# Optimization experiments

Hardware: AMD Instinct MI355X
Metric: run time of the kernel (lower is better)

## Reference

```python
import jax, jax.numpy as jnp
import numpy as np

ALPHA = 0.2  # LeakyReLU negative slope


def setup_inputs() -> dict:
    key = jax.random.key(0)
    ks = jax.random.split(key, 6)
    B, N, F_IN, F_OUT = 4, 4096, 128, 128
    return {
        "input": jax.random.normal(ks[0], (B, N, F_IN), dtype=jnp.float32),
        "adj": jax.random.uniform(ks[1], (B, N, N), dtype=jnp.float32),
        "W": jax.random.normal(ks[2], (F_IN, F_OUT), dtype=jnp.float32) * (np.sqrt(2.0) / np.sqrt(F_IN)),
        "a1": jax.random.normal(ks[3], (F_OUT, 1), dtype=jnp.float32) * 0.1,
        "a2": jax.random.normal(ks[4], (F_OUT, 1), dtype=jnp.float32) * 0.1,
        "bias": jax.random.normal(ks[5], (N, F_OUT), dtype=jnp.float32) * 0.02,
    }


def reference(input, adj, W, a1, a2, bias):
    # h = X @ W : [B, N, F_out]
    h = jnp.einsum("bnf,fo->bno", input, W)
    # additive attention scores: e[b,i,j] = leakyrelu(f1[b,i] + f2[b,j])
    f1 = h @ a1            # [B, N, 1]
    f2 = h @ a2            # [B, N, 1]
    e = f1 + jnp.swapaxes(f2, 1, 2)        # [B, N, N]
    e = jnp.where(e >= 0, e, ALPHA * e)    # LeakyReLU
    # NOTE: original multiplies adj into scores (not -inf masking) and
    # softmaxes over dim=1 (the first node axis), faithfully reproduced.
    attention = jax.nn.softmax(adj * e, axis=1)  # [B, N, N]
    # dropout p=0 / eval mode -> identity
    h_prime = jnp.einsum("bij,bjo->bio", attention, h) + bias[None, :, :]
    # in_features == out_features -> plain residual
    return h_prime + input
```

## Files before the change

kernel.cpp:

```cpp
#include <hip/hip_runtime.h>
#include <hip/hip_bf16.h>

typedef short short8 __attribute__((ext_vector_type(8)));
typedef float f32x4 __attribute__((ext_vector_type(4)));
typedef unsigned short u16;
typedef u16 u16x4 __attribute__((ext_vector_type(4)));
typedef u16 u16x8 __attribute__((ext_vector_type(8)));

static constexpr float kAlpha = 0.2f;

static __device__ inline u16 f2bf(float f) {
  __hip_bfloat16 h = __float2bfloat16(f);
  return *reinterpret_cast<u16*>(&h);
}
static __device__ inline float bf2f(u16 v) {
  unsigned int u = ((unsigned int)v) << 16;
  return __uint_as_float(u);
}

__global__ __launch_bounds__(256) void k1_hW(const float* __restrict__ X,
                                             const float* __restrict__ W,
                                             const float* __restrict__ a1,
                                             const float* __restrict__ a2,
                                             u16* __restrict__ hbT,
                                             float* __restrict__ f1,
                                             float* __restrict__ f2) {
  int row0 = blockIdx.x * 8;
  int o = threadIdx.x & 127;
  int g = threadIdx.x >> 7;
  __shared__ float Xs[8][128];
#pragma unroll
  for (int s = 0; s < 4; ++s) {
    int idx = threadIdx.x + s * 256;
    Xs[idx >> 7][idx & 127] = X[(size_t)row0 * 128 + idx];
  }
  __syncthreads();
  float acc[4] = {0.f, 0.f, 0.f, 0.f};
  for (int k = 0; k < 128; ++k) {
    float w = W[k * 128 + o];
#pragma unroll
    for (int s = 0; s < 4; ++s) acc[s] += Xs[g + 2 * s][k] * w;
  }
  int b = row0 >> 12;
  int n0 = row0 & 4095;
#pragma unroll
  for (int s = 0; s < 4; ++s)
    hbT[((size_t)b * 128 + o) * 4096 + n0 + g + 2 * s] = f2bf(acc[s]);

  float a1o = a1[o], a2o = a2[o];
  __syncthreads();
#pragma unroll
  for (int s = 0; s < 4; ++s) Xs[g + 2 * s][o] = acc[s] * a1o;
  __syncthreads();
  int r = threadIdx.x >> 5, c = threadIdx.x & 31;
  float s1 = Xs[r][c] + Xs[r][c + 32] + Xs[r][c + 64] + Xs[r][c + 96];
  s1 += __shfl_xor(s1, 1);
  s1 += __shfl_xor(s1, 2);
  s1 += __shfl_xor(s1, 4);
  s1 += __shfl_xor(s1, 8);
  s1 += __shfl_xor(s1, 16);
  if (c == 0) f1[b * 4096 + n0 + r] = s1;
  __syncthreads();
#pragma unroll
  for (int s = 0; s < 4; ++s) Xs[g + 2 * s][o] = acc[s] * a2o;
  __syncthreads();
  float s2 = Xs[r][c] + Xs[r][c + 32] + Xs[r][c + 64] + Xs[r][c + 96];
  s2 += __shfl_xor(s2, 1);
  s2 += __shfl_xor(s2, 2);
  s2 += __shfl_xor(s2, 4);
  s2 += __shfl_xor(s2, 8);
  s2 += __shfl_xor(s2, 16);
  if (c == 0) f2[b * 4096 + n0 + r] = s2;
}

__global__ __launch_bounds__(256) void k2_dpart(const float* __restrict__ adj,
                                                const float* __restrict__ f1,
                                                const float* __restrict__ f2,
                                                float* __restrict__ dpart) {
  int bid = blockIdx.x;
  int ic = bid & 31;
  int jt = (bid >> 5) & 15;
  int b = bid >> 9;
  int t = threadIdx.x;
  int c = t & 63, r = t >> 6;
  int j = jt * 256 + c * 4;
  const size_t badj = (size_t)b * 4096 * 4096;
  f32x4 f2v = *reinterpret_cast<const f32x4*>(&f2[b * 4096 + j]);
  const float* f1p = f1 + b * 4096;
  int row0 = ic * 128 + r;
  f32x4 sum = (f32x4){0.f, 0.f, 0.f, 0.f};
#pragma unroll 8
  for (int s = 0; s < 32; ++s) {
    int row = row0 + 4 * s;
    f32x4 a = *reinterpret_cast<const f32x4*>(&adj[badj + (size_t)row * 4096 + j]);
    float f1r = f1p[row];
#pragma unroll
    for (int k = 0; k < 4; ++k) {
      float e = f1r + f2v[k];
      e = e >= 0.f ? e : kAlpha * e;
      sum[k] += __expf(a[k] * e);
    }
  }
  __shared__ f32x4 red[256];
  red[t] = sum;
  __syncthreads();
  if (t < 64) {
    f32x4 tt = red[t] + red[t + 64] + red[t + 128] + red[t + 192];
    *reinterpret_cast<f32x4*>(&dpart[(size_t)(b * 32 + ic) * 4096 + j]) = tt;
  }
}

#define LROWW 72
#define BARRIER()                                      \
  {                                                    \
    asm volatile("s_waitcnt lgkmcnt(0)" ::: "memory"); \
    __builtin_amdgcn_s_barrier();                      \
  }
__global__ __launch_bounds__(512) void k3w(const float* __restrict__ adj,
                                           const u16* __restrict__ hbT,
                                           const float* __restrict__ f1,
                                           const float* __restrict__ f2,
                                           const float* __restrict__ dpart,
                                           u16* __restrict__ parts) {
  int bid0 = blockIdx.x;
  int bid = ((bid0 & 7) << 5) | (bid0 >> 3);
  int b = bid >> 6;
  int it = (bid >> 2) & 15;
  int jq = bid & 3;
  int i0 = it * 256;
  int jbase = jq * 1024;
  int t = threadIdx.x;
  int lane = t & 63;
  int w = t >> 6;
  int rw = w & 3;
  int cw = w >> 2;

  __shared__ u16 As[2][256 * LROWW];
  __shared__ u16 Bs[2][128 * LROWW];
  __shared__ float rds[1024];

  const size_t badj = (size_t)b * 4096 * 4096;
  const u16* hb = hbT + (size_t)b * 128 * 4096;
  const float* f2b = f2 + b * 4096;

  int r0 = t >> 4;
  int c0 = (t & 15) * 4;
  int bo = t >> 2;
  int bc0 = (t & 3) * 16;

  float f1v[8];
#pragma unroll
  for (int u = 0; u < 8; ++u) f1v[u] = f1[b * 4096 + i0 + r0 + 32 * u];

  int l15 = lane & 15;
  int l8 = (lane >> 4) * 8;

  f32x4 acc[4][4];
#pragma unroll
  for (int rg = 0; rg < 4; ++rg)
#pragma unroll
    for (int n = 0; n < 4; ++n) acc[rg][n] = (f32x4){0.f, 0.f, 0.f, 0.f};

  const float* ap0 = adj + badj + (size_t)(i0 + r0) * 4096 + c0;

  f32x4 raA0, raA1, raA2, raA3, raA4, raA5, raA6, raA7;
  f32x4 raB0, raB1, raB2, raB3, raB4, raB5, raB6, raB7;
  f32x4 rfA, rfB;
  u16x8 rbA0, rbA1, rbB0, rbB1;

#define PF(S, JO)                                                         \
  {                                                                       \
    int jj = jbase + ((JO) & 1023);    \
    const float* ap = ap0 + jj;                                           \
    ra##S##0 = *reinterpret_cast<const f32x4*>(ap);                       \
    ra##S##1 = *reinterpret_cast<const f32x4*>(ap + (size_t)1 * 131072);  \
    ra##S##2 = *reinterpret_cast<const f32x4*>(ap + (size_t)2 * 131072);  \
    ra##S##3 = *reinterpret_cast<const f32x4*>(ap + (size_t)3 * 131072);  \
    ra##S##4 = *reinterpret_cast<const f32x4*>(ap + (size_t)4 * 131072);  \
    ra##S##5 = *reinterpret_cast<const f32x4*>(ap + (size_t)5 * 131072);  \
    ra##S##6 = *reinterpret_cast<const f32x4*>(ap + (size_t)6 * 131072);  \
    ra##S##7 = *reinterpret_cast<const f32x4*>(ap + (size_t)7 * 131072);  \
    rf##S = *reinterpret_cast<const f32x4*>(f2b + jj + c0);               \
    const u16* bp = hb + (size_t)bo * 4096 + jj + bc0;                    \
    rb##S##0 = *reinterpret_cast<const u16x8*>(bp);                       \
    rb##S##1 = *reinterpret_cast<const u16x8*>(bp + 8);                   \
  }

#define STU(S, U, BUF)                                                    \
  {                                                                       \
    u16x4 pv;                                                             \
    _Pragma("unroll") for (int k = 0; k < 4; ++k) {                       \
      float e = f1v[U] + rf##S[k];                                        \
      e = e >= 0.f ? e : kAlpha * e;                                      \
      pv[k] = f2bf(__expf(ra##S##U[k] * e) * rdv[k]);                     \
    }                                                                     \
    *reinterpret_cast<u16x4*>(&As[BUF][(r0 + 32 * U) * LROWW + c0]) = pv; \
  }

#define STORE(S, BUF, JO)                                                 \
  {                                                                       \
    f32x4 rdv = *reinterpret_cast<const f32x4*>(&rds[((JO) & 1023) + c0]);\
    STU(S, 0, BUF) STU(S, 1, BUF) STU(S, 2, BUF) STU(S, 3, BUF)           \
    STU(S, 4, BUF) STU(S, 5, BUF) STU(S, 6, BUF) STU(S, 7, BUF)           \
    *reinterpret_cast<u16x8*>(&Bs[BUF][bo * LROWW + bc0]) = rb##S##0;     \
    *reinterpret_cast<u16x8*>(&Bs[BUF][bo * LROWW + bc0 + 8]) = rb##S##1; \
  }

#define DOMFMA(BUF)                                                                \
  {                                                                                \
    _Pragma("unroll") for (int kk = 0; kk < 64; kk += 32) {                        \
      short8 af0 = *reinterpret_cast<const short8*>(                               \
          &As[BUF][(rw * 64 + 0 * 16 + l15) * LROWW + kk + l8]);                   \
      short8 af1 = *reinterpret_cast<const short8*>(                               \
          &As[BUF][(rw * 64 + 1 * 16 + l15) * LROWW + kk + l8]);                   \
      short8 af2 = *reinterpret_cast<const short8*>(                               \
          &As[BUF][(rw * 64 + 2 * 16 + l15) * LROWW + kk + l8]);                   \
      short8 af3 = *reinterpret_cast<const short8*>(                               \
          &As[BUF][(rw * 64 + 3 * 16 + l15) * LROWW + kk + l8]);                   \
      _Pragma("unroll") for (int n = 0; n < 4; ++n) {                              \
        short8 bf = *reinterpret_cast<const short8*>(                              \
            &Bs[BUF][(cw * 64 + n * 16 + l15) * LROWW + kk + l8]);                 \
        acc[0][n] = __builtin_amdgcn_mfma_f32_16x16x32_bf16(af0, bf, acc[0][n], 0, 0, 0); \
        acc[1][n] = __builtin_amdgcn_mfma_f32_16x16x32_bf16(af1, bf, acc[1][n], 0, 0, 0); \
        acc[2][n] = __builtin_amdgcn_mfma_f32_16x16x32_bf16(af2, bf, acc[2][n], 0, 0, 0); \
        acc[3][n] = __builtin_amdgcn_mfma_f32_16x16x32_bf16(af3, bf, acc[3][n], 0, 0, 0); \
      }                                                                            \
    }                                                                              \
  }

  PF(A, 0);
  PF(B, 64);

  {
    const float* dp = dpart + (size_t)b * 32 * 4096 + jbase;
#pragma unroll
    for (int u = 0; u < 2; ++u) {
      int jj = t * 2 + u;
      float s = 0.f;
#pragma unroll
      for (int ic = 0; ic < 32; ++ic) s += dp[(size_t)ic * 4096 + jj];
      rds[jj] = 1.0f / s;
    }
  }
  __syncthreads();

  for (int j0 = 0; j0 < 1024; j0 += 128) {
    STORE(A, 0, j0);
    BARRIER();
    DOMFMA(0);
    PF(A, j0 + 128);
    STORE(B, 1, j0 + 64);
    BARRIER();
    DOMFMA(1);
    PF(B, j0 + 192);
  }

  u16* pq = parts + (size_t)(b * 4 + jq) * 4096 * 128;
#pragma unroll
  for (int rg = 0; rg < 4; ++rg) {
#pragma unroll
    for (int n = 0; n < 4; ++n) {
      int o = cw * 64 + n * 16 + l15;
#pragma unroll
      for (int q = 0; q < 4; ++q) {
        int i = i0 + rw * 64 + rg * 16 + (lane >> 4) * 4 + q;
        pq[(size_t)i * 128 + o] = f2bf(acc[rg][n][q]);
      }
    }
  }
}

__global__ __launch_bounds__(256) void k4r(const u16* __restrict__ parts,
                                           const float* __restrict__ bias,
                                           const float* __restrict__ input,
                                           float* __restrict__ out) {
  size_t v = (size_t)blockIdx.x * 256 + threadIdx.x;
  int b = (int)(v >> 17);
  size_t e = (v & 131071) * 4;
  const u16* pb = parts + (size_t)b * 4 * 524288;
  u16x4 p0 = *reinterpret_cast<const u16x4*>(&pb[e]);
  u16x4 p1 = *reinterpret_cast<const u16x4*>(&pb[e + 524288]);
  u16x4 p2 = *reinterpret_cast<const u16x4*>(&pb[e + 2 * 524288]);
  u16x4 p3 = *reinterpret_cast<const u16x4*>(&pb[e + 3 * 524288]);
  f32x4 bv = *reinterpret_cast<const f32x4*>(&bias[e]);
  size_t ge = (size_t)b * 524288 + e;
  f32x4 iv = *reinterpret_cast<const f32x4*>(&input[ge]);
  f32x4 s;
#pragma unroll
  for (int k = 0; k < 4; ++k)
    s[k] = bf2f(p0[k]) + bf2f(p1[k]) + bf2f(p2[k]) + bf2f(p3[k]) + bv[k] + iv[k];
  *reinterpret_cast<f32x4*>(&out[ge]) = s;
}

extern "C" void kernel_launch(void* const* d_in, const int* in_sizes, int n_in,
                              void* d_out, int out_size, void* d_ws, size_t ws_size,
                              hipStream_t stream) {
  const float* input = (const float*)d_in[0];
  const float* adj = (const float*)d_in[1];
  const float* W = (const float*)d_in[2];
  const float* a1 = (const float*)d_in[3];
  const float* a2 = (const float*)d_in[4];
  const float* bias = (const float*)d_in[5];
  float* out = (float*)d_out;

  char* ws = (char*)d_ws;
  u16* hbT = (u16*)(ws);
  float* f1 = (float*)(ws + 4194304);
  float* f2 = (float*)(ws + 4259840);
  float* dpart = (float*)(ws + 4325376);
  u16* parts = (u16*)(ws + 6422528);

  k1_hW<<<2048, 256, 0, stream>>>(input, W, a1, a2, hbT, f1, f2);
  k2_dpart<<<2048, 256, 0, stream>>>(adj, f1, f2, dpart);
  k3w<<<256, 512, 0, stream>>>(adj, hbT, f1, f2, dpart, parts);
  k4r<<<2048, 256, 0, stream>>>(parts, bias, input, out);
}
```

Before: 134.2 us.

## Split attention kernels per batch so adj slice stays cache-resident between passes

Launches the denominator and weighted-sum kernels once per batch instead of over all batches, so each batch's adjacency slice may be reused from the large last-level cache by the second pass. The main kernel's row tile shrinks from 256 to 64 rows to keep 256 blocks per launch, and the denominator kernel uses 512-thread blocks. The aim is to remove the second full HBM read of adj, at the cost of more launches, more redundant hbT tile loads and less MFMA reuse per block.

```diff
diff --git a/kernel.cpp b/kernel.cpp
--- a/kernel.cpp
+++ b/kernel.cpp
@@ -73,27 +73,24 @@
   if (c == 0) f2[b * 4096 + n0 + r] = s2;
 }
 
-__global__ __launch_bounds__(256) void k2_dpart(const float* __restrict__ adj,
-                                                const float* __restrict__ f1,
-                                                const float* __restrict__ f2,
+__global__ __launch_bounds__(512) void k2_dpart(const float* __restrict__ adjb,
+                                                const float* __restrict__ f1b,
+                                                const float* __restrict__ f2b,
                                                 float* __restrict__ dpart) {
   int bid = blockIdx.x;
   int ic = bid & 31;
-  int jt = (bid >> 5) & 15;
-  int b = bid >> 9;
+  int jt = bid >> 5;
   int t = threadIdx.x;
   int c = t & 63, r = t >> 6;
   int j = jt * 256 + c * 4;
-  const size_t badj = (size_t)b * 4096 * 4096;
-  f32x4 f2v = *reinterpret_cast<const f32x4*>(&f2[b * 4096 + j]);
-  const float* f1p = f1 + b * 4096;
+  f32x4 f2v = *reinterpret_cast<const f32x4*>(&f2b[j]);
   int row0 = ic * 128 + r;
   f32x4 sum = (f32x4){0.f, 0.f, 0.f, 0.f};
 #pragma unroll 8
-  for (int s = 0; s < 32; ++s) {
-    int row = row0 + 4 * s;
-    f32x4 a = *reinterpret_cast<const f32x4*>(&adj[badj + (size_t)row * 4096 + j]);
-    float f1r = f1p[row];
+  for (int s = 0; s < 16; ++s) {
+    int row = row0 + 8 * s;
+    f32x4 a = *reinterpret_cast<const f32x4*>(&adjb[(size_t)row * 4096 + j]);
+    float f1r = f1b[row];
 #pragma unroll
     for (int k = 0; k < 4; ++k) {
       float e = f1r + f2v[k];
@@ -101,12 +98,14 @@
       sum[k] += __expf(a[k] * e);
     }
   }
-  __shared__ f32x4 red[256];
+  __shared__ f32x4 red[512];
   red[t] = sum;
   __syncthreads();
   if (t < 64) {
-    f32x4 tt = red[t] + red[t + 64] + red[t + 128] + red[t + 192];
-    *reinterpret_cast<f32x4*>(&dpart[(size_t)(b * 32 + ic) * 4096 + j]) = tt;
+    f32x4 tt = red[t];
+#pragma unroll
+    for (int m = 1; m < 8; ++m) tt += red[t + 64 * m];
+    *reinterpret_cast<f32x4*>(&dpart[(size_t)ic * 4096 + j]) = tt;
   }
 }
 
@@ -116,18 +115,17 @@
     asm volatile("s_waitcnt lgkmcnt(0)" ::: "memory"); \
     __builtin_amdgcn_s_barrier();                      \
   }
-__global__ __launch_bounds__(512) void k3w(const float* __restrict__ adj,
-                                           const u16* __restrict__ hbT,
-                                           const float* __restrict__ f1,
-                                           const float* __restrict__ f2,
+__global__ __launch_bounds__(512) void k3w(const float* __restrict__ adjb,
+                                           const u16* __restrict__ hbTb,
+                                           const float* __restrict__ f1b,
+                                           const float* __restrict__ f2b,
                                            const float* __restrict__ dpart,
-                                           u16* __restrict__ parts) {
+                                           u16* __restrict__ partsb) {
   int bid0 = blockIdx.x;
   int bid = ((bid0 & 7) << 5) | (bid0 >> 3);
-  int b = bid >> 6;
-  int it = (bid >> 2) & 15;
+  int it = bid >> 2;
   int jq = bid & 3;
-  int i0 = it * 256;
+  int i0 = it * 64;
   int jbase = jq * 1024;
   int t = threadIdx.x;
   int lane = t & 63;
@@ -135,55 +133,42 @@
   int rw = w & 3;
   int cw = w >> 2;
 
-  __shared__ u16 As[2][256 * LROWW];
+  __shared__ u16 As[2][64 * LROWW];
   __shared__ u16 Bs[2][128 * LROWW];
   __shared__ float rds[1024];
-
-  const size_t badj = (size_t)b * 4096 * 4096;
-  const u16* hb = hbT + (size_t)b * 128 * 4096;
-  const float* f2b = f2 + b * 4096;
 
   int r0 = t >> 4;
   int c0 = (t & 15) * 4;
   int bo = t >> 2;
   int bc0 = (t & 3) * 16;
 
-  float f1v[8];
-#pragma unroll
-  for (int u = 0; u < 8; ++u) f1v[u] = f1[b * 4096 + i0 + r0 + 32 * u];
+  float f1v[2];
+#pragma unroll
+  for (int u = 0; u < 2; ++u) f1v[u] = f1b[i0 + r0 + 32 * u];
 
   int l15 = lane & 15;
   int l8 = (lane >> 4) * 8;
 
-  f32x4 acc[4][4];
-#pragma unroll
-  for (int rg = 0; rg < 4; ++rg)
-#pragma unroll
-    for (int n = 0; n < 4; ++n) acc[rg][n] = (f32x4){0.f, 0.f, 0.f, 0.f};
-
-  const float* ap0 = adj + badj + (size_t)(i0 + r0) * 4096 + c0;
-
-  f32x4 raA0, raA1, raA2, raA3, raA4, raA5, raA6, raA7;
-  f32x4 raB0, raB1, raB2, raB3, raB4, raB5, raB6, raB7;
+  f32x4 acc[4];
+#pragma unroll
+  for (int n = 0; n < 4; ++n) acc[n] = (f32x4){0.f, 0.f, 0.f, 0.f};
+
+  const float* ap0 = adjb + (size_t)(i0 + r0) * 4096 + c0;
+
+  f32x4 raA0, raA1, raB0, raB1;
   f32x4 rfA, rfB;
   u16x8 rbA0, rbA1, rbB0, rbB1;
 
-#define PF(S, JO)                                                         \
-  {                                                                       \
-    int jj = jbase + ((JO) & 1023);    \
-    const float* ap = ap0 + jj;                                           \
-    ra##S##0 = *reinterpret_cast<const f32x4*>(ap);                       \
-    ra##S##1 = *reinterpret_cast<const f32x4*>(ap + (size_t)1 * 131072);  \
-    ra##S##2 = *reinterpret_cast<const f32x4*>(ap + (size_t)2 * 131072);  \
-    ra##S##3 = *reinterpret_cast<const f32x4*>(ap + (size_t)3 * 131072);  \
-    ra##S##4 = *reinterpret_cast<const f32x4*>(ap + (size_t)4 * 131072);  \
-    ra##S##5 = *reinterpret_cast<const f32x4*>(ap + (size_t)5 * 131072);  \
-    ra##S##6 = *reinterpret_cast<const f32x4*>(ap + (size_t)6 * 131072);  \
-    ra##S##7 = *reinterpret_cast<const f32x4*>(ap + (size_t)7 * 131072);  \
-    rf##S = *reinterpret_cast<const f32x4*>(f2b + jj + c0);               \
-    const u16* bp = hb + (size_t)bo * 4096 + jj + bc0;                    \
-    rb##S##0 = *reinterpret_cast<const u16x8*>(bp);                       \
-    rb##S##1 = *reinterpret_cast<const u16x8*>(bp + 8);                   \
+#define PF(S, JO)                                                        \
+  {                                                                      \
+    int jj = jbase + ((JO) & 1023);   \
+    const float* ap = ap0 + jj;                                          \
+    ra##S##0 = *reinterpret_cast<const f32x4*>(ap);                      \
+    ra##S##1 = *reinterpret_cast<const f32x4*>(ap + (size_t)32 * 4096);  \
+    rf##S = *reinterpret_cast<const f32x4*>(f2b + jj + c0);              \
+    const u16* bp = hbTb + (size_t)bo * 4096 + jj + bc0;                 \
+    rb##S##0 = *reinterpret_cast<const u16x8*>(bp);                      \
+    rb##S##1 = *reinterpret_cast<const u16x8*>(bp + 8);                  \
   }
 
 #define STU(S, U, BUF)                                                    \
@@ -197,33 +182,23 @@
     *reinterpret_cast<u16x4*>(&As[BUF][(r0 + 32 * U) * LROWW + c0]) = pv; \
   }
 
-#define STORE(S, BUF, JO)                                                 \
-  {                                                                       \
-    f32x4 rdv = *reinterpret_cast<const f32x4*>(&rds[((JO) & 1023) + c0]);\
-    STU(S, 0, BUF) STU(S, 1, BUF) STU(S, 2, BUF) STU(S, 3, BUF)           \
-    STU(S, 4, BUF) STU(S, 5, BUF) STU(S, 6, BUF) STU(S, 7, BUF)           \
-    *reinterpret_cast<u16x8*>(&Bs[BUF][bo * LROWW + bc0]) = rb##S##0;     \
-    *reinterpret_cast<u16x8*>(&Bs[BUF][bo * LROWW + bc0 + 8]) = rb##S##1; \
+#define STORE(S, BUF, JO)                                                  \
+  {                                                                        \
+    f32x4 rdv = *reinterpret_cast<const f32x4*>(&rds[((JO) & 1023) + c0]); \
+    STU(S, 0, BUF) STU(S, 1, BUF)                                          \
+    *reinterpret_cast<u16x8*>(&Bs[BUF][bo * LROWW + bc0]) = rb##S##0;      \
+    *reinterpret_cast<u16x8*>(&Bs[BUF][bo * LROWW + bc0 + 8]) = rb##S##1;  \
   }
 
 #define DOMFMA(BUF)                                                                \
   {                                                                                \
     _Pragma("unroll") for (int kk = 0; kk < 64; kk += 32) {                        \
-      short8 af0 = *reinterpret_cast<const short8*>(                               \
-          &As[BUF][(rw * 64 + 0 * 16 + l15) * LROWW + kk + l8]);                   \
-      short8 af1 = *reinterpret_cast<const short8*>(                               \
-          &As[BUF][(rw * 64 + 1 * 16 + l15) * LROWW + kk + l8]);                   \
-      short8 af2 = *reinterpret_cast<const short8*>(                               \
-          &As[BUF][(rw * 64 + 2 * 16 + l15) * LROWW + kk + l8]);                   \
-      short8 af3 = *reinterpret_cast<const short8*>(                               \
-          &As[BUF][(rw * 64 + 3 * 16 + l15) * LROWW + kk + l8]);                   \
+      short8 af = *reinterpret_cast<const short8*>(                                \
+          &As[BUF][(rw * 16 + l15) * LROWW + kk + l8]);                            \
       _Pragma("unroll") for (int n = 0; n < 4; ++n) {                              \
         short8 bf = *reinterpret_cast<const short8*>(                              \
             &Bs[BUF][(cw * 64 + n * 16 + l15) * LROWW + kk + l8]);                 \
-        acc[0][n] = __builtin_amdgcn_mfma_f32_16x16x32_bf16(af0, bf, acc[0][n], 0, 0, 0); \
-        acc[1][n] = __builtin_amdgcn_mfma_f32_16x16x32_bf16(af1, bf, acc[1][n], 0, 0, 0); \
-        acc[2][n] = __builtin_amdgcn_mfma_f32_16x16x32_bf16(af2, bf, acc[2][n], 0, 0, 0); \
-        acc[3][n] = __builtin_amdgcn_mfma_f32_16x16x32_bf16(af3, bf, acc[3][n], 0, 0, 0); \
+        acc[n] = __builtin_amdgcn_mfma_f32_16x16x32_bf16(af, bf, acc[n], 0, 0, 0); \
       }                                                                            \
     }                                                                              \
   }
@@ -232,15 +207,16 @@
   PF(B, 64);
 
   {
-    const float* dp = dpart + (size_t)b * 32 * 4096 + jbase;
-#pragma unroll
-    for (int u = 0; u < 2; ++u) {
-      int jj = t * 2 + u;
-      float s = 0.f;
-#pragma unroll
-      for (int ic = 0; ic < 32; ++ic) s += dp[(size_t)ic * 4096 + jj];
-      rds[jj] = 1.0f / s;
+    const float* dp = dpart + jbase;
+    int jj = t * 2;
+    float s0 = 0.f, s1 = 0.f;
+#pragma unroll
+    for (int ic = 0; ic < 32; ++ic) {
+      s0 += dp[(size_t)ic * 4096 + jj];
+      s1 += dp[(size_t)ic * 4096 + jj + 1];
     }
+    rds[jj] = 1.0f / s0;
+    rds[jj + 1] = 1.0f / s1;
   }
   __syncthreads();
 
@@ -255,17 +231,14 @@
     PF(B, j0 + 192);
   }
 
-  u16* pq = parts + (size_t)(b * 4 + jq) * 4096 * 128;
-#pragma unroll
-  for (int rg = 0; rg < 4; ++rg) {
-#pragma unroll
-    for (int n = 0; n < 4; ++n) {
-      int o = cw * 64 + n * 16 + l15;
-#pragma unroll
-      for (int q = 0; q < 4; ++q) {
-        int i = i0 + rw * 64 + rg * 16 + (lane >> 4) * 4 + q;
-        pq[(size_t)i * 128 + o] = f2bf(acc[rg][n][q]);
-      }
+  u16* pq = partsb + (size_t)jq * 4096 * 128;
+#pragma unroll
+  for (int n = 0; n < 4; ++n) {
+    int o = cw * 64 + n * 16 + l15;
+#pragma unroll
+    for (int q = 0; q < 4; ++q) {
+      int i = i0 + rw * 16 + (lane >> 4) * 4 + q;
+      pq[(size_t)i * 128 + o] = f2bf(acc[n][q]);
     }
   }
 }
@@ -311,7 +284,14 @@
   u16* parts = (u16*)(ws + 6422528);
 
   k1_hW<<<2048, 256, 0, stream>>>(input, W, a1, a2, hbT, f1, f2);
-  k2_dpart<<<2048, 256, 0, stream>>>(adj, f1, f2, dpart);
-  k3w<<<256, 512, 0, stream>>>(adj, hbT, f1, f2, dpart, parts);
+  for (int b = 0; b < 4; ++b) {
+    const float* adjb = adj + (size_t)b * 4096 * 4096;
+    const float* f1b = f1 + b * 4096;
+    const float* f2b = f2 + b * 4096;
+    const u16* hbTb = hbT + (size_t)b * 128 * 4096;
+    u16* partsb = parts + (size_t)b * 4 * 4096 * 128;
+    k2_dpart<<<512, 512, 0, stream>>>(adjb, f1b, f2b, dpart);
+    k3w<<<256, 512, 0, stream>>>(adjb, hbTb, f1b, f2b, dpart, partsb);
+  }
   k4r<<<2048, 256, 0, stream>>>(parts, bias, input, out);
 }
```

After: 178.1 us. +32.7%, slower.
